# Kernel tuning notes

Measured on AMD Instinct MI355X. Metric: run time of the kernel, lower is better.

The kernel has to match this reference:

```python
import jax, jax.numpy as jnp
import numpy as np
import math

B, N, M, H = 4, 1024, 1024, 512
EPS = 1e-5


def _ln(x, g, b):
    m = jnp.mean(x, axis=-1, keepdims=True)
    v = jnp.mean((x - m) ** 2, axis=-1, keepdims=True)
    return (x - m) * jax.lax.rsqrt(v + EPS) * g + b


def _heads(x, h):
    b, s, Hh = x.shape
    return x.reshape(b, s, h, Hh // h).transpose(0, 2, 1, 3)  # [b,h,s,d]


def _merge(x):
    b, h, s, d = x.shape
    return x.transpose(0, 2, 1, 3).reshape(b, s, h * d)


def _sdpa(q, k, v):
    d = q.shape[-1]
    a = jax.nn.softmax(jnp.einsum('bhqd,bhkd->bhqk', q, k) / math.sqrt(d), axis=-1)
    return jnp.einsum('bhqk,bhkd->bhqd', a, v)


def _attn(key, value, query, Wk, Wv, Wq, Wf, bf, g, b, h):
    residual = query
    K = _heads(key @ Wk, h)
    V = _heads(value @ Wv, h)
    Q = _heads(query @ Wq, h)
    r = _merge(_sdpa(Q, K, V))
    r = jnp.concatenate([residual, r], axis=-1) @ Wf + bf
    return _ln(r + residual, g, b)


def _sc_attn(x, x2, Wk, Wv, Wq, Wf, bf, g, b, h=2):
    residual = x
    sK, sV, sQ = _heads(x @ Wk, h), _heads(x @ Wv, h), _heads(x @ Wq, h)
    cK, cV, cQ = _heads(x2 @ Wk, h), _heads(x2 @ Wv, h), _heads(x2 @ Wq, h)
    r = _sdpa(sQ, sK, sV) + _sdpa(cQ, cK, cV) + _sdpa(cQ, sK, sV) + _sdpa(sQ, cK, cV)
    r = _merge(r)
    r = jnp.concatenate([residual, r], axis=-1) @ Wf + bf
    return _ln(r + residual, g, b)


def _forward(context_x, context_y, target_x, in_W, in_b, cx_W, cx_b, tx_W, tx_b,
             sc_Wk, sc_Wv, sc_Wq, sc_Wf, sc_bf, sc_g, sc_b,
             ca_Wk, ca_Wv, ca_Wq, ca_Wf, ca_bf, ca_g, ca_b):
    bsz = context_x.shape[0]
    y = context_y.reshape(bsz, -1, 4, 2)
    proj = lambda yd: jnp.concatenate([context_x, yd], axis=-1) @ in_W + in_b
    e = proj(y[:, :, 0, :])
    e1 = proj(y[:, :, 1, :])
    e2 = proj(y[:, :, 2, :])
    e3 = proj(y[:, :, 3, :])
    # first self pass: key2/value2/query2 == current encoder_input
    for i in range(2):
        e = _sc_attn(e, e, sc_Wk[i], sc_Wv[i], sc_Wq[i], sc_Wf[i], sc_bf[i], sc_g[i], sc_b[i])
    for x2 in (e1, e2, e3):
        for i in range(2):
            e = _sc_attn(e, x2, sc_Wk[i], sc_Wv[i], sc_Wq[i], sc_Wf[i], sc_bf[i], sc_g[i], sc_b[i])
    q = target_x @ tx_W + tx_b
    k = context_x @ cx_W + cx_b
    for i in range(2):
        q = _attn(k, e, q, ca_Wk[i], ca_Wv[i], ca_Wq[i], ca_Wf[i], ca_bf[i], ca_g[i], ca_b[i], h=4)
    return q


def setup_inputs() -> dict:
    key = jax.random.key(0)
    ks = jax.random.split(key, 24)
    w = lambda i, shape, s: jax.random.normal(ks[i], shape, jnp.float32) * s
    return {
        'context_x': jax.random.normal(ks[0], (B, N, 1), jnp.float32),
        'context_y': jax.random.normal(ks[1], (B, N, 8), jnp.float32),
        'target_x': jax.random.normal(ks[2], (B, M, 1), jnp.float32),
        'in_W': w(3, (3, H), 0.5), 'in_b': jnp.zeros((H,), jnp.float32),
        'cx_W': w(4, (1, H), 0.5), 'cx_b': jnp.zeros((H,), jnp.float32),
        'tx_W': w(5, (1, H), 0.5), 'tx_b': jnp.zeros((H,), jnp.float32),
        'sc_Wk': w(6, (2, H, H), 0.03), 'sc_Wv': w(7, (2, H, H), 0.03), 'sc_Wq': w(8, (2, H, H), 0.03),
        'sc_Wf': w(9, (2, 2 * H, H), 0.03), 'sc_bf': jnp.zeros((2, H), jnp.float32),
        'sc_g': jnp.ones((2, H), jnp.float32), 'sc_b': jnp.zeros((2, H), jnp.float32),
        'ca_Wk': w(10, (2, H, H), 0.03), 'ca_Wv': w(11, (2, H, H), 0.03), 'ca_Wq': w(12, (2, H, H), 0.03),
        'ca_Wf': w(13, (2, 2 * H, H), 0.03), 'ca_bf': jnp.zeros((2, H), jnp.float32),
        'ca_g': jnp.ones((2, H), jnp.float32), 'ca_b': jnp.zeros((2, H), jnp.float32),
    }


def reference(context_x, context_y, target_x, in_W, in_b, cx_W, cx_b, tx_W, tx_b,
              sc_Wk, sc_Wv, sc_Wq, sc_Wf, sc_bf, sc_g, sc_b,
              ca_Wk, ca_Wv, ca_Wq, ca_Wf, ca_bf, ca_g, ca_b):
    return _forward(context_x, context_y, target_x, in_W, in_b, cx_W, cx_b, tx_W, tx_b,
                    sc_Wk, sc_Wv, sc_Wq, sc_Wf, sc_bf, sc_g, sc_b,
                    ca_Wk, ca_Wv, ca_Wq, ca_Wf, ca_bf, ca_g, ca_b)
```

## Files before the change

kernel.cpp:

```cpp
#include <hip/hip_runtime.h>

#define DEVINL __device__ __forceinline__

typedef short bf16x8 __attribute__((ext_vector_type(8)));
typedef float f32x4 __attribute__((ext_vector_type(4)));

#define LOG2E 1.44269504088896f

DEVINL unsigned f2b(float f) {
  unsigned u = __float_as_uint(f);
  u = (u + 0x7FFFu + ((u >> 16) & 1u)) >> 16;
  return u & 0xFFFFu;
}
DEVINL uint4 pack8(const float* v) {
  uint4 u;
  u.x = f2b(v[0]) | (f2b(v[1]) << 16);
  u.y = f2b(v[2]) | (f2b(v[3]) << 16);
  u.z = f2b(v[4]) | (f2b(v[5]) << 16);
  u.w = f2b(v[6]) | (f2b(v[7]) << 16);
  return u;
}

DEVINL float4 block_sum4(float4 v, float4* sh) {
  const int lane = threadIdx.x & 63, wid = threadIdx.x >> 6;
#pragma unroll
  for (int o = 32; o; o >>= 1) {
    v.x += __shfl_down(v.x, o);
    v.y += __shfl_down(v.y, o);
    v.z += __shfl_down(v.z, o);
    v.w += __shfl_down(v.w, o);
  }
  __syncthreads();
  if (lane == 0) sh[wid] = v;
  __syncthreads();
  float4 a = sh[0], b = sh[1], c = sh[2], d = sh[3], r;
  r.x = a.x + b.x + c.x + d.x;
  r.y = a.y + b.y + c.y + d.y;
  r.z = a.z + b.z + c.z + d.z;
  r.w = a.w + b.w + c.w + d.w;
  return r;
}
DEVINL float block_sum1(float v, float* sh) {
  const int lane = threadIdx.x & 63, wid = threadIdx.x >> 6;
#pragma unroll
  for (int o = 32; o; o >>= 1) v += __shfl_down(v, o);
  __syncthreads();
  if (lane == 0) sh[wid] = v;
  __syncthreads();
  return sh[0] + sh[1] + sh[2] + sh[3];
}

__global__ __launch_bounds__(256) void tabproj9_kernel(
    const float* __restrict__ in_W, const float* __restrict__ in_b,
    const float* __restrict__ cx_W, const float* __restrict__ cx_b,
    const float* __restrict__ tx_W, const float* __restrict__ tx_b,
    const float* __restrict__ sWk, const float* __restrict__ sWv,
    const float* __restrict__ sWq, const float* __restrict__ aWk,
    const float* __restrict__ aWq, float* __restrict__ Ttab) {
  const int z = blockIdx.y;
  const float* V;
  const float* bias;
  const float* W;
  float* P;
  int nvec;
  float scl = 1.f;
  if (z < 6) {
    V = in_W; bias = in_b; nvec = 3;
    const int i = z / 3, wsel = z % 3;
    W = (wsel == 0 ? sWk : wsel == 1 ? sWv : sWq) + (size_t)i * 262144;
    P = Ttab + (size_t)z * 2048;
    if (wsel == 2) scl = 0.0625f * LOG2E;
  } else if (z < 8) {
    V = cx_W; bias = cx_b; nvec = 1;
    W = aWk + (size_t)(z - 6) * 262144;
    P = Ttab + 12288 + (size_t)(z - 6) * 1024;
  } else {
    V = tx_W; bias = tx_b; nvec = 1;
    W = aWq; P = Ttab + 14336; scl = 0.08838834764831845f * LOG2E;
  }
  __shared__ float4 sh4[4];
  const int j = blockIdx.x, tid = threadIdx.x;
  float acc[4] = {0.f, 0.f, 0.f, 0.f};
  for (int kk = tid; kk < 512; kk += 256) {
    const float w = W[(size_t)kk * 512 + j];
    for (int v = 0; v < nvec; ++v) acc[v] += V[(size_t)v * 512 + kk] * w;
    acc[3] += bias[kk] * w;
  }
  float4 packed = make_float4(acc[0], acc[1], acc[2], acc[3]);
  packed = block_sum4(packed, sh4);
  if (tid == 0) {
    const float vals[4] = {packed.x * scl, packed.y * scl, packed.z * scl, packed.w * scl};
    for (int v = 0; v < nvec; ++v) P[(size_t)v * 512 + j] = vals[v];
    P[(size_t)nvec * 512 + j] = vals[3];
  }
}

__global__ __launch_bounds__(256) void transpose_kvq_kernel(
    const float* __restrict__ sWk, const float* __restrict__ sWv,
    const float* __restrict__ sWq, const float* __restrict__ aWv,
    const float* __restrict__ aWq, unsigned short* __restrict__ Wkvqt0,
    unsigned short* __restrict__ aWvt0, unsigned short* __restrict__ aWqt1) {
  const int z = blockIdx.z;
  const float* src;
  unsigned short* dst;
  float scl = 1.f;
  if (z < 6) {
    const int i = z / 3, wsel = z % 3;
    src = (wsel == 0 ? sWk : wsel == 1 ? sWv : sWq) + (size_t)i * 262144;
    dst = Wkvqt0 + (size_t)i * 786432 + (size_t)wsel * 262144;
    if (wsel == 2) scl = 0.0625f * LOG2E;
  } else if (z < 8) {
    src = aWv + (size_t)(z - 6) * 262144;
    dst = aWvt0 + (size_t)(z - 6) * 262144;
  } else {
    src = aWq + 262144; dst = aWqt1; scl = 0.08838834764831845f * LOG2E;
  }
  __shared__ float tile[32][33];
  const int n0 = blockIdx.x * 32, k0 = blockIdx.y * 32;
  const int tx = threadIdx.x, ty = threadIdx.y;
#pragma unroll
  for (int r = 0; r < 4; ++r)
    tile[ty + 8 * r][tx] = src[(size_t)(k0 + ty + 8 * r) * 512 + n0 + tx];
  __syncthreads();
#pragma unroll
  for (int r = 0; r < 4; ++r)
    dst[(size_t)(n0 + ty + 8 * r) * 512 + k0 + tx] =
        (unsigned short)f2b(scl * tile[tx][ty + 8 * r]);
}

__global__ __launch_bounds__(256) void transpose_f_kernel(
    const float* __restrict__ sWf, const float* __restrict__ aWf,
    unsigned short* __restrict__ Wft0, unsigned short* __restrict__ aWft0) {
  const int z = blockIdx.z;
  const float* src = (z < 2 ? sWf + (size_t)z * 524288 : aWf + (size_t)(z - 2) * 524288);
  unsigned short* dst =
      (z < 2 ? Wft0 + (size_t)z * 524288 : aWft0 + (size_t)(z - 2) * 524288);
  __shared__ float tile[32][33];
  const int n0 = blockIdx.x * 32, k0 = blockIdx.y * 32;
  const int tx = threadIdx.x, ty = threadIdx.y;
#pragma unroll
  for (int r = 0; r < 4; ++r)
    tile[ty + 8 * r][tx] = src[(size_t)(k0 + ty + 8 * r) * 512 + n0 + tx];
  __syncthreads();
#pragma unroll
  for (int r = 0; r < 4; ++r)
    dst[(size_t)(n0 + ty + 8 * r) * 1024 + k0 + tx] =
        (unsigned short)f2b(tile[tx][ty + 8 * r]);
}

__global__ __launch_bounds__(128) void affine3kq_kernel(
    const float* __restrict__ cx, const float* __restrict__ cy, int sel,
    const float* __restrict__ TK, const float* __restrict__ TQ,
    unsigned short* __restrict__ Kfr, unsigned short* __restrict__ Qbf) {
  const int row = blockIdx.x;
  const int b = row >> 10, s = row & 1023;
  const float x = cx[row];
  const float* y = cy + (size_t)row * 8 + 2 * sel;
  const float y0 = y[0], y1 = y[1];
  const int t = threadIdx.x;
  const bool isQ = t >= 64;
  const int c = t & 63;
  const int h = c >> 5;
  const int d0 = (c & 31) * 8;
  const float* T = isQ ? TQ : TK;
  float v[8];
#pragma unroll
  for (int j = 0; j < 8; ++j) {
    const int col = h * 256 + d0 + j;
    v[j] = x * T[col] + y0 * T[512 + col] + y1 * T[1024 + col] + T[1536 + col];
  }
  const uint4 u = pack8(v);
  const int bh = b * 2 + h;
  if (isQ) {
    *(uint4*)(Qbf + ((size_t)bh * 1024 + s) * 256 + d0) = u;
  } else {
    const int kc = d0 >> 5;
    const int lane = ((d0 & 31) >> 3) * 16 + (s & 15);
    *(uint4*)(Kfr + ((size_t)(bh * 8 + kc) * 64 + (s >> 4)) * 512 + lane * 8) = u;
  }
}

__global__ __launch_bounds__(256) void affine3v_frag_kernel(
    const float* __restrict__ cx, const float* __restrict__ cy, int sel,
    const float* __restrict__ TV, unsigned short* __restrict__ Vfr) {
  __shared__ float tile[32][33];
  const int s0 = blockIdx.x * 32, d0 = blockIdx.y * 32;
  const int bh = blockIdx.z;
  const int b = bh >> 1, h = bh & 1;
  const int tx = threadIdx.x, ty = threadIdx.y;
  const int col = h * 256 + d0 + tx;
  const float tv0 = TV[col], tv1 = TV[512 + col], tv2 = TV[1024 + col],
              tv3 = TV[1536 + col];
#pragma unroll
  for (int r = 0; r < 4; ++r) {
    const int row = b * 1024 + s0 + ty + 8 * r;
    const float x = cx[row];
    const float* y = cy + (size_t)row * 8 + 2 * sel;
    tile[ty + 8 * r][tx] = x * tv0 + y[0] * tv1 + y[1] * tv2 + tv3;
  }
  __syncthreads();
  const int idx = ty * 32 + tx;
  if (idx < 128) {
    const int dj = idx & 31, sch = idx >> 5;
    float v[8];
#pragma unroll
    for (int jj = 0; jj < 8; ++jj) v[jj] = tile[sch * 8 + jj][dj];
    const uint4 u = pack8(v);
    const int sc = s0 >> 5;
    const int dtile = (d0 + dj) >> 4;
    const int lane = sch * 16 + (dj & 15);
    *(uint4*)(Vfr + ((size_t)(bh * 32 + sc) * 16 + dtile) * 512 + lane * 8) = u;
  }
}

__global__ __launch_bounds__(64) void rank1_pack_kernel(
    const float* __restrict__ x, const float* __restrict__ T,
    unsigned short* __restrict__ dst, int isQ) {
  const int row = blockIdx.x;
  const int b = row >> 10, s = row & 1023;
  const float xv = x[row];
  const int c = threadIdx.x;
  const int h = c >> 4;
  const int d0 = (c & 15) * 8;
  float v[8];
#pragma unroll
  for (int j = 0; j < 8; ++j) {
    const int col = h * 128 + d0 + j;
    v[j] = xv * T[col] + T[512 + col];
  }
  const uint4 u = pack8(v);
  const int bh = b * 4 + h;
  if (isQ) {
    *(uint4*)(dst + ((size_t)bh * 1024 + s) * 128 + d0) = u;
  } else {
    const int kc = d0 >> 5;
    const int lane = ((d0 & 31) >> 3) * 16 + (s & 15);
    *(uint4*)(dst + ((size_t)(bh * 4 + kc) * 64 + (s >> 4)) * 512 + lane * 8) = u;
  }
}

__global__ __launch_bounds__(512) void affine3_kernel(
    const float* __restrict__ cx, const float* __restrict__ cy, int sel,
    const float* __restrict__ W3, const float* __restrict__ bias,
    float* __restrict__ out, unsigned short* __restrict__ outb) {
  const int r = blockIdx.x, j = threadIdx.x;
  const float* y = cy + (size_t)r * 8 + 2 * sel;
  const float v = cx[r] * W3[j] + y[0] * W3[512 + j] + y[1] * W3[1024 + j] + bias[j];
  if (out) out[(size_t)r * 512 + j] = v;
  if (outb) outb[(size_t)r * 512 + j] = (unsigned short)f2b(v);
}

__global__ __launch_bounds__(512) void rank1_kernel(
    const float* __restrict__ x, const float* __restrict__ w,
    const float* __restrict__ b, float* __restrict__ out,
    unsigned short* __restrict__ outb) {
  const int r = blockIdx.x, j = threadIdx.x;
  const float v = x[r] * w[j] + b[j];
  if (out) out[(size_t)r * 512 + j] = v;
  if (outb) outb[(size_t)r * 512 + j] = (unsigned short)f2b(v);
}

__global__ __launch_bounds__(256) void gemm_wf_kernel(
    const unsigned short* __restrict__ A0, const unsigned short* __restrict__ A1,
    const float* __restrict__ F0, const float* __restrict__ F1,
    const unsigned short* __restrict__ Wt, const float* __restrict__ bias,
    float* __restrict__ C0, float* __restrict__ C1) {
  constexpr int BM = 128, BN = 64, BK = 32, LDP = 40, K = 512, N = 512;
  __shared__ unsigned short As[2][BM * LDP];
  __shared__ unsigned short Bs[2][BN * LDP];
  const int kz = blockIdx.z;
  const int tid = threadIdx.x;
  const int lane = tid & 63, w = tid >> 6;
  const int bm = blockIdx.y * BM, bn = blockIdx.x * BN;
  const int wm = (w & 1) * 64, wn = (w >> 1) * 32;
  const int l15 = lane & 15, lq = lane >> 4;
  const int ar = tid >> 1, ac = (tid & 1) * 16;
  const int br = tid >> 2, bc = (tid & 3) * 8;
  const unsigned short* A = kz ? A1 : A0;
  const bool useF = (kz != 0) && (F0 != nullptr);
  const size_t arow = (size_t)(bm + ar) * 512;
  const size_t brow = (size_t)(bn + br) * 1024 + (size_t)kz * 512;
  f32x4 acc[4][2] = {};
  uint4 ra0, ra1, rb0;
#define GLOAD(k0_)                                                          \
  do {                                                                      \
    if (useF) {                                                             \
      const float* p0 = F0 + arow + (k0_) + ac;                             \
      const float* p1 = F1 + arow + (k0_) + ac;                             \
      float s[16];                                                          \
      const float4 x0 = *(const float4*)p0, x1 = *(const float4*)(p0 + 4);  \
      const float4 x2 = *(const float4*)(p0 + 8), x3 = *(const float4*)(p0 + 12); \
      const float4 y0 = *(const float4*)p1, y1 = *(const float4*)(p1 + 4);  \
      const float4 y2 = *(const float4*)(p1 + 8), y3 = *(const float4*)(p1 + 12); \
      s[0] = x0.x + y0.x; s[1] = x0.y + y0.y; s[2] = x0.z + y0.z; s[3] = x0.w + y0.w; \
      s[4] = x1.x + y1.x; s[5] = x1.y + y1.y; s[6] = x1.z + y1.z; s[7] = x1.w + y1.w; \
      s[8] = x2.x + y2.x; s[9] = x2.y + y2.y; s[10] = x2.z + y2.z; s[11] = x2.w + y2.w; \
      s[12] = x3.x + y3.x; s[13] = x3.y + y3.y; s[14] = x3.z + y3.z; s[15] = x3.w + y3.w; \
      ra0 = pack8(s); ra1 = pack8(s + 8);                                   \
    } else {                                                                \
      ra0 = *(const uint4*)(A + arow + (k0_) + ac);                         \
      ra1 = *(const uint4*)(A + arow + (k0_) + ac + 8);                     \
    }                                                                       \
    rb0 = *(const uint4*)(Wt + brow + (k0_) + bc);                          \
  } while (0)
  GLOAD(0);
  *(uint4*)(As[0] + ar * LDP + ac) = ra0;
  *(uint4*)(As[0] + ar * LDP + ac + 8) = ra1;
  *(uint4*)(Bs[0] + br * LDP + bc) = rb0;
  __syncthreads();
  int buf = 0;
  for (int k0 = 0; k0 < K; k0 += BK) {
    const bool more = (k0 + BK) < K;
    if (more) GLOAD(k0 + BK);
    bf16x8 af[4], bfr[2];
#pragma unroll
    for (int mt = 0; mt < 4; ++mt)
      af[mt] = *(const bf16x8*)(As[buf] + (wm + mt * 16 + l15) * LDP + lq * 8);
#pragma unroll
    for (int nt = 0; nt < 2; ++nt)
      bfr[nt] = *(const bf16x8*)(Bs[buf] + (wn + nt * 16 + l15) * LDP + lq * 8);
#pragma unroll
    for (int mt = 0; mt < 4; ++mt)
#pragma unroll
      for (int nt = 0; nt < 2; ++nt)
        acc[mt][nt] =
            __builtin_amdgcn_mfma_f32_16x16x32_bf16(af[mt], bfr[nt], acc[mt][nt], 0, 0, 0);
    if (more) {
      *(uint4*)(As[buf ^ 1] + ar * LDP + ac) = ra0;
      *(uint4*)(As[buf ^ 1] + ar * LDP + ac + 8) = ra1;
      *(uint4*)(Bs[buf ^ 1] + br * LDP + bc) = rb0;
    }
    __syncthreads();
    buf ^= 1;
  }
#undef GLOAD
  float* C = kz ? C1 : C0;
#pragma unroll
  for (int nt = 0; nt < 2; ++nt) {
    const int col = bn + wn + nt * 16 + l15;
    const float bv = (kz && bias) ? bias[col] : 0.f;
#pragma unroll
    for (int mt = 0; mt < 4; ++mt) {
#pragma unroll
      for (int r = 0; r < 4; ++r) {
        const int row = bm + wm + mt * 16 + lq * 4 + r;
        C[(size_t)row * N + col] = acc[mt][nt][r] + bv;
      }
    }
  }
}

template <int MODE>
__global__ __launch_bounds__(256) void gemm_pack_kernel(
    const unsigned short* __restrict__ A0, const unsigned short* __restrict__ Wt,
    unsigned short* __restrict__ Kfr, unsigned short* __restrict__ Vfr,
    unsigned short* __restrict__ Qbf) {
  constexpr int BM = 128, BN = 64, BK = 32, LDP = 40, K = 512;
  __shared__ unsigned short As[2][BM * LDP];
  __shared__ unsigned short Bs[2][BN * LDP];
  const int tid = threadIdx.x;
  const int lane = tid & 63, w = tid >> 6;
  const int bm = blockIdx.y * BM, bn = blockIdx.x * BN;
  const int wm = (w & 1) * 64, wn = (w >> 1) * 32;
  const int l15 = lane & 15, lq = lane >> 4;
  const int ar = tid >> 1, ac = (tid & 1) * 16;
  const int br = tid >> 2, bc = (tid & 3) * 8;
  f32x4 acc[4][2] = {};
  uint4 ra0 = *(const uint4*)(A0 + (size_t)(bm + ar) * K + ac);
  uint4 ra1 = *(const uint4*)(A0 + (size_t)(bm + ar) * K + ac + 8);
  uint4 rb0 = *(const uint4*)(Wt + (size_t)(bn + br) * K + bc);
  *(uint4*)(As[0] + ar * LDP + ac) = ra0;
  *(uint4*)(As[0] + ar * LDP + ac + 8) = ra1;
  *(uint4*)(Bs[0] + br * LDP + bc) = rb0;
  __syncthreads();
  int buf = 0;
  for (int k0 = 0; k0 < K; k0 += BK) {
    const bool more = (k0 + BK) < K;
    if (more) {
      ra0 = *(const uint4*)(A0 + (size_t)(bm + ar) * K + k0 + BK + ac);
      ra1 = *(const uint4*)(A0 + (size_t)(bm + ar) * K + k0 + BK + ac + 8);
      rb0 = *(const uint4*)(Wt + (size_t)(bn + br) * K + k0 + BK + bc);
    }
    bf16x8 af[4], bfr[2];
#pragma unroll
    for (int mt = 0; mt < 4; ++mt)
      af[mt] = *(const bf16x8*)(As[buf] + (wm + mt * 16 + l15) * LDP + lq * 8);
#pragma unroll
    for (int nt = 0; nt < 2; ++nt)
      bfr[nt] = *(const bf16x8*)(Bs[buf] + (wn + nt * 16 + l15) * LDP + lq * 8);
#pragma unroll
    for (int mt = 0; mt < 4; ++mt)
#pragma unroll
      for (int nt = 0; nt < 2; ++nt)
        acc[mt][nt] =
            __builtin_amdgcn_mfma_f32_16x16x32_bf16(af[mt], bfr[nt], acc[mt][nt], 0, 0, 0);
    if (more) {
      *(uint4*)(As[buf ^ 1] + ar * LDP + ac) = ra0;
      *(uint4*)(As[buf ^ 1] + ar * LDP + ac + 8) = ra1;
      *(uint4*)(Bs[buf ^ 1] + br * LDP + bc) = rb0;
    }
    __syncthreads();
    buf ^= 1;
  }
  const int b = bm >> 10;
  const int s0base = (bm & 1023) + wm + lq * 4;
#pragma unroll
  for (int nt = 0; nt < 2; ++nt) {
    const int col = bn + wn + nt * 16 + l15;
    int sec, h, d, nh2, Dv;
    if constexpr (MODE == 0) {
      sec = col >> 9; const int c = col & 511; h = c >> 8; d = c & 255; nh2 = 2; Dv = 256;
    } else if constexpr (MODE == 1) {
      sec = 1; h = col >> 7; d = col & 127; nh2 = 4; Dv = 128;
    } else {
      sec = 2; h = col >> 7; d = col & 127; nh2 = 4; Dv = 128;
    }
    const int bh = b * nh2 + h;
#pragma unroll
    for (int mt = 0; mt < 4; ++mt) {
      const int s0 = s0base + mt * 16;
      const float* a = (const float*)&acc[mt][nt];
      if (sec == 2) {
        unsigned short* q = Qbf + ((size_t)bh * 1024 + s0) * Dv + d;
#pragma unroll
        for (int r = 0; r < 4; ++r) q[(size_t)r * Dv] = (unsigned short)f2b(a[r]);
      } else if (sec == 0) {
        unsigned short* kp = Kfr +
            ((size_t)(bh * 8 + (d >> 5)) * 64 + (s0 >> 4)) * 512 +
            ((d & 31) >> 3) * 128 + (d & 7);
#pragma unroll
        for (int r = 0; r < 4; ++r)
          kp[((s0 & 15) + r) * 8] = (unsigned short)f2b(a[r]);
      } else {
        unsigned short* vp = Vfr +
            ((size_t)(bh * 32 + (s0 >> 5)) * (Dv / 16) + (d >> 4)) * 512 +
            (((s0 >> 3) & 3) * 16 + (d & 15)) * 8 + (s0 & 7);
        uint2 u;
        u.x = f2b(a[0]) | (f2b(a[1]) << 16);
        u.y = f2b(a[2]) | (f2b(a[3]) << 16);
        *(uint2*)vp = u;
      }
    }
  }
}

template <int D, int NKV>
__global__ __launch_bounds__(256, 2) void attn_mfma_kernel(
    const unsigned short* __restrict__ Qa, const unsigned short* __restrict__ Qb,
    const unsigned short* __restrict__ KfrA, const unsigned short* __restrict__ KfrB,
    const unsigned short* __restrict__ VfrA, const unsigned short* __restrict__ VfrB,
    float post_scale, int nh, unsigned short* __restrict__ R,
    float* __restrict__ Rp) {
  constexpr int NQS = NKV;
  constexpr int QP = D + 8;
  constexpr int WPh = 512 + 8;
  constexpr int DT = D / 64;
  const int tid = threadIdx.x;
  const int lane = tid & 63, w = tid >> 6;
  const int l15 = lane & 15, lq = lane >> 4;
  const int nbh = 4 * nh;
  int bx = blockIdx.x;
  int side = 0;
  if constexpr (NKV == 2) { side = bx >> 9; bx &= 511; }
  const int bh = bx % nbh;
  const int qb16 = (bx / nbh) * 16;
  const int b = bh / nh, head = bh % nh;
  const size_t rowb = (size_t)b * 1024;
  const int colo = head * D;

  __shared__ unsigned short qsh[NQS * 16 * QP];
  __shared__ unsigned short wsh[16 * WPh];
  __shared__ float redA[4][16];
  __shared__ float redB[4][16];

  for (int idx = tid; idx < NQS * 16 * (D / 8); idx += 256) {
    const int st = idx / (16 * (D / 8));
    const int rem = idx - st * 16 * (D / 8);
    const int r = rem / (D / 8), ch = rem - r * (D / 8);
    const unsigned short* Q = st ? Qb : Qa;
    const uint4 u = *(const uint4*)(Q + ((size_t)bh * 1024 + qb16 + r) * D + ch * 8);
    *(uint4*)(qsh + st * 16 * QP + r * QP + ch * 8) = u;
  }
  __syncthreads();

  const unsigned short* Kp = (side ? KfrB : KfrA) + (size_t)bh * ((size_t)D * 1024);
  const unsigned short* Vp = (side ? VfrB : VfrA) + (size_t)bh * ((size_t)D * 1024);

  f32x4 acc[NQS][16] = {};
#pragma unroll 1
  for (int kc = 0; kc < D / 32; ++kc) {
    bf16x8 kf[16];
#pragma unroll
    for (int st = 0; st < 16; ++st)
      kf[st] = *(const bf16x8*)(Kp + ((size_t)kc * 64 + w * 16 + st) * 512 + lane * 8);
    const bf16x8 qa = *(const bf16x8*)(qsh + l15 * QP + kc * 32 + lq * 8);
    __builtin_amdgcn_s_setprio(1);
#pragma unroll
    for (int st = 0; st < 16; ++st)
      acc[0][st] = __builtin_amdgcn_mfma_f32_16x16x32_bf16(qa, kf[st], acc[0][st], 0, 0, 0);
    __builtin_amdgcn_s_setprio(0);
    if constexpr (NQS == 2) {
      const bf16x8 qb2 = *(const bf16x8*)(qsh + 16 * QP + l15 * QP + kc * 32 + lq * 8);
      __builtin_amdgcn_s_setprio(1);
#pragma unroll
      for (int st = 0; st < 16; ++st)
        acc[1][st] =
            __builtin_amdgcn_mfma_f32_16x16x32_bf16(qb2, kf[st], acc[1][st], 0, 0, 0);
      __builtin_amdgcn_s_setprio(0);
    }
  }

  float psA[4] = {0.f, 0.f, 0.f, 0.f}, psB[4] = {0.f, 0.f, 0.f, 0.f};
#pragma unroll
  for (int st = 0; st < 16; ++st)
#pragma unroll
    for (int r = 0; r < 4; ++r) {
      acc[0][st][r] = exp2f(acc[0][st][r]);
      psA[r] += acc[0][st][r];
      if constexpr (NQS == 2) {
        acc[1][st][r] = exp2f(acc[1][st][r]);
        psB[r] += acc[1][st][r];
      }
    }
#pragma unroll
  for (int o = 1; o < 16; o <<= 1)
#pragma unroll
    for (int r = 0; r < 4; ++r) {
      psA[r] += __shfl_xor(psA[r], o);
      if constexpr (NQS == 2) psB[r] += __shfl_xor(psB[r], o);
    }
  if (l15 == 0) {
#pragma unroll
    for (int r = 0; r < 4; ++r) {
      redA[w][lq * 4 + r] = psA[r];
      if constexpr (NQS == 2) redB[w][lq * 4 + r] = psB[r];
    }
  }
  __syncthreads();
  float invA[4], invB[4];
#pragma unroll
  for (int r = 0; r < 4; ++r) {
    invA[r] = 1.f / (redA[0][lq * 4 + r] + redA[1][lq * 4 + r] +
                     redA[2][lq * 4 + r] + redA[3][lq * 4 + r]);
    if constexpr (NQS == 2)
      invB[r] = 1.f / (redB[0][lq * 4 + r] + redB[1][lq * 4 + r] +
                       redB[2][lq * 4 + r] + redB[3][lq * 4 + r]);
  }

  f32x4 acc_o[DT] = {};
#pragma unroll
  for (int half = 0; half < 2; ++half) {
#pragma unroll
    for (int st = 0; st < 8; ++st) {
      const int g = half * 8 + st;
#pragma unroll
      for (int r = 0; r < 4; ++r) {
        float wv = acc[0][g][r] * invA[r];
        if constexpr (NQS == 2) wv += acc[1][g][r] * invB[r];
        wsh[(lq * 4 + r) * WPh + w * 128 + st * 16 + l15] = (unsigned short)f2b(wv);
      }
    }
    __syncthreads();
#pragma unroll 1
    for (int sh2 = 0; sh2 < 16; sh2 += 2) {
      bf16x8 pa[2], vb[2][DT];
#pragma unroll
      for (int u = 0; u < 2; ++u) {
        const int sc = sh2 + u;
        pa[u] = *(const bf16x8*)(wsh + l15 * WPh + sc * 32 + lq * 8);
        const int scg = (sc >> 2) * 8 + half * 4 + (sc & 3);
#pragma unroll
        for (int dt = 0; dt < DT; ++dt)
          vb[u][dt] = *(const bf16x8*)(
              Vp + ((size_t)scg * (D / 16) + w * DT + dt) * 512 + lane * 8);
      }
      __builtin_amdgcn_s_setprio(1);
#pragma unroll
      for (int u = 0; u < 2; ++u)
#pragma unroll
        for (int dt = 0; dt < DT; ++dt)
          acc_o[dt] =
              __builtin_amdgcn_mfma_f32_16x16x32_bf16(pa[u], vb[u][dt], acc_o[dt], 0, 0, 0);
      __builtin_amdgcn_s_setprio(0);
    }
    __syncthreads();
  }

  if constexpr (NKV == 2) {
    float* dst = Rp + (size_t)side * (4096 * 512) + (rowb + qb16) * 512 + colo;
#pragma unroll
    for (int dt = 0; dt < DT; ++dt)
#pragma unroll
      for (int r = 0; r < 4; ++r) {
        const int q = lq * 4 + r;
        const int d = w * (DT * 16) + dt * 16 + l15;
        dst[(size_t)q * 512 + d] = acc_o[dt][r];
      }
  } else {
#pragma unroll
    for (int dt = 0; dt < DT; ++dt)
#pragma unroll
      for (int r = 0; r < 4; ++r) {
        const int q = lq * 4 + r;
        const int d = w * (DT * 16) + dt * 16 + l15;
        R[(rowb + qb16 + q) * 512 + colo + d] =
            (unsigned short)f2b(acc_o[dt][r] * post_scale);
      }
  }
}

__global__ __launch_bounds__(256) void ln_kernel(
    const float* __restrict__ G0, const float* __restrict__ G1,
    const float* __restrict__ res, const float* __restrict__ g,
    const float* __restrict__ b, float* __restrict__ out,
    unsigned short* __restrict__ outb) {
  __shared__ float sh[4];
  const int row = blockIdx.x, tid = threadIdx.x;
  const size_t off = (size_t)row * 512;
  const float x0 = G0[off + tid] + G1[off + tid] + res[off + tid];
  const float x1 = G0[off + tid + 256] + G1[off + tid + 256] + res[off + tid + 256];
  const float mean = block_sum1(x0 + x1, sh) * (1.0f / 512.0f);
  const float d0 = x0 - mean, d1 = x1 - mean;
  const float var = block_sum1(d0 * d0 + d1 * d1, sh) * (1.0f / 512.0f);
  const float inv = rsqrtf(var + 1e-5f);
  const float y0 = d0 * inv * g[tid] + b[tid];
  const float y1 = d1 * inv * g[tid + 256] + b[tid + 256];
  out[off + tid] = y0;
  out[off + tid + 256] = y1;
  if (outb) {
    outb[off + tid] = (unsigned short)f2b(y0);
    outb[off + tid + 256] = (unsigned short)f2b(y1);
  }
}

extern "C" void kernel_launch(void* const* d_in, const int* in_sizes, int n_in,
                              void* d_out, int out_size, void* d_ws, size_t ws_size,
                              hipStream_t stream) {
  typedef unsigned short ushort_t;
  const float* cx   = (const float*)d_in[0];
  const float* cy   = (const float*)d_in[1];
  const float* txp  = (const float*)d_in[2];
  const float* in_W = (const float*)d_in[3];
  const float* in_b = (const float*)d_in[4];
  const float* cx_W = (const float*)d_in[5];
  const float* cx_b = (const float*)d_in[6];
  const float* tx_W = (const float*)d_in[7];
  const float* tx_b = (const float*)d_in[8];
  const float* sWk  = (const float*)d_in[9];
  const float* sWv  = (const float*)d_in[10];
  const float* sWq  = (const float*)d_in[11];
  const float* sWf  = (const float*)d_in[12];
  const float* sbf  = (const float*)d_in[13];
  const float* sg   = (const float*)d_in[14];
  const float* sb   = (const float*)d_in[15];
  const float* aWk  = (const float*)d_in[16];
  const float* aWv  = (const float*)d_in[17];
  const float* aWq  = (const float*)d_in[18];
  const float* aWf  = (const float*)d_in[19];
  const float* abf  = (const float*)d_in[20];
  const float* ag   = (const float*)d_in[21];
  const float* ab   = (const float*)d_in[22];

  const size_t MB = 1024 * 1024;
  char* ws = (char*)d_ws;
  float*    E     = (float*)(ws + 0 * MB);
  ushort_t* Ebf   = (ushort_t*)(ws + 8 * MB);
  float*    QA    = (float*)(ws + 12 * MB);
  ushort_t* QAbf  = (ushort_t*)(ws + 20 * MB);
  ushort_t* Rbbf  = (ushort_t*)(ws + 24 * MB);
  float*    Rp    = (float*)(ws + 28 * MB);
  float*    G0    = (float*)(ws + 44 * MB);
  ushort_t* KfrA  = (ushort_t*)(ws + 52 * MB);
  ushort_t* VfrA  = (ushort_t*)(ws + 56 * MB);
  ushort_t* QbfA  = (ushort_t*)(ws + 60 * MB);
  ushort_t* KfrB  = (ushort_t*)(ws + 64 * MB);
  ushort_t* VfrB  = (ushort_t*)(ws + 68 * MB);
  ushort_t* QbfB  = (ushort_t*)(ws + 72 * MB);
  float*    G1    = (float*)(ws + 84 * MB);
  ushort_t* Wkvqt0 = (ushort_t*)(ws + 92 * MB);
  ushort_t* Wkvqt[2] = {Wkvqt0, Wkvqt0 + 786432};
  ushort_t* Wft0   = (ushort_t*)(ws + 95 * MB);
  ushort_t* Wft[2] = {Wft0, Wft0 + 524288};
  ushort_t* aWvt0  = (ushort_t*)(ws + 97 * MB);
  ushort_t* aWvt[2] = {aWvt0, aWvt0 + 262144};
  ushort_t* aWqt1  = (ushort_t*)(ws + 98 * MB);
  ushort_t* aWft0  = (ushort_t*)(ws + 99 * MB);
  ushort_t* aWft[2] = {aWft0, aWft0 + 524288};
  float*    Ttab   = (float*)(ws + 101 * MB);

  float* T_sc[2][3];
  for (int i = 0; i < 2; ++i)
    for (int w = 0; w < 3; ++w) T_sc[i][w] = Ttab + (size_t)(i * 3 + w) * 2048;
  float* T_cak[2] = {Ttab + 12288, Ttab + 12288 + 1024};
  float* T_caq0 = Ttab + 14336;

  const dim3 tb(32, 8);

  transpose_kvq_kernel<<<dim3(16, 16, 9), tb, 0, stream>>>(sWk, sWv, sWq, aWv, aWq,
                                                           Wkvqt0, aWvt0, aWqt1);
  transpose_f_kernel<<<dim3(16, 32, 4), tb, 0, stream>>>(sWf, aWf, Wft0, aWft0);
  tabproj9_kernel<<<dim3(512, 9), 256, 0, stream>>>(in_W, in_b, cx_W, cx_b, tx_W, tx_b,
                                                    sWk, sWv, sWq, aWk, aWq, Ttab);

  affine3_kernel<<<4096, 512, 0, stream>>>(cx, cy, 0, in_W, in_b, E, Ebf);
  rank1_kernel<<<4096, 512, 0, stream>>>(txp, tx_W, tx_b, QA, QAbf);

  for (int p = 0; p < 4; ++p) {
    for (int i = 0; i < 2; ++i) {
      gemm_pack_kernel<0><<<dim3(24, 32), 256, 0, stream>>>(Ebf, Wkvqt[i], KfrA, VfrA,
                                                            QbfA);
      const float* F0 = nullptr;
      const float* F1 = nullptr;
      if (p > 0) {
        affine3kq_kernel<<<4096, 128, 0, stream>>>(cx, cy, p, T_sc[i][0], T_sc[i][2],
                                                   KfrB, QbfB);
        affine3v_frag_kernel<<<dim3(32, 8, 8), tb, 0, stream>>>(cx, cy, p, T_sc[i][1],
                                                                VfrB);
        attn_mfma_kernel<256, 2><<<1024, 256, 0, stream>>>(
            QbfA, QbfB, KfrA, KfrB, VfrA, VfrB, 1.0f, 2, nullptr, Rp);
        F0 = Rp; F1 = Rp + 4096 * 512;
      } else {
        attn_mfma_kernel<256, 1><<<512, 256, 0, stream>>>(
            QbfA, QbfA, KfrA, KfrA, VfrA, VfrA, 4.0f, 2, Rbbf, nullptr);
      }
      gemm_wf_kernel<<<dim3(8, 32, 2), 256, 0, stream>>>(
          Ebf, Rbbf, F0, F1, Wft[i], sbf + (size_t)i * 512, G0, G1);
      ln_kernel<<<4096, 256, 0, stream>>>(G0, G1, E, sg + (size_t)i * 512,
                                          sb + (size_t)i * 512, E, Ebf);
    }
  }

  for (int i = 0; i < 2; ++i) {
    rank1_pack_kernel<<<4096, 64, 0, stream>>>(cx, T_cak[i], KfrA, 0);
    gemm_pack_kernel<1><<<dim3(8, 32), 256, 0, stream>>>(Ebf, aWvt[i], nullptr, VfrA,
                                                         nullptr);
    if (i == 0) {
      rank1_pack_kernel<<<4096, 64, 0, stream>>>(txp, T_caq0, QbfB, 1);
    } else {
      gemm_pack_kernel<2><<<dim3(8, 32), 256, 0, stream>>>(QAbf, aWqt1, nullptr, nullptr,
                                                           QbfB);
    }
    attn_mfma_kernel<128, 1><<<1024, 256, 0, stream>>>(
        QbfB, QbfB, KfrA, KfrA, VfrA, VfrA, 1.0f, 4, Rbbf, nullptr);
    gemm_wf_kernel<<<dim3(8, 32, 2), 256, 0, stream>>>(
        QAbf, Rbbf, nullptr, nullptr, aWft[i], abf + (size_t)i * 512, G0, G1);
    ln_kernel<<<4096, 256, 0, stream>>>(G0, G1, QA, ag + (size_t)i * 512,
                                        ab + (size_t)i * 512,
                                        (i == 1) ? (float*)d_out : QA,
                                        (i == 1) ? nullptr : QAbf);
  }
  (void)in_sizes; (void)n_in; (void)out_size; (void)ws_size;
}
```

Measured before the change: 1.064 ms.

## Restructure attention kernel into key-chunked loop with multi-tile query reuse

The attention kernel now walks the 1024 keys in four chunks, computing scores, exponentials and the P·V product per chunk. Probabilities are staged unnormalized in shared memory and normalized once at the end. The full score accumulator no longer has to stay in registers, and a new QT template parameter lets each block handle several 16-row query tiles, so each loaded K/V fragment is reused across more queries. In the two-side case the normalized outputs are summed in registers, and grid sizes are halved to match. The cost is more shared memory, more barriers per block, and fewer blocks in flight.

New measurement: 1.029 ms. 3.3% less time.

```diff
diff --git a/kernel.cpp b/kernel.cpp
--- a/kernel.cpp
+++ b/kernel.cpp
@@ -444,168 +444,185 @@
   }
 }
 
-template <int D, int NKV>
+template <int D, int NQS, int QT>
 __global__ __launch_bounds__(256, 2) void attn_mfma_kernel(
     const unsigned short* __restrict__ Qa, const unsigned short* __restrict__ Qb,
     const unsigned short* __restrict__ KfrA, const unsigned short* __restrict__ KfrB,
     const unsigned short* __restrict__ VfrA, const unsigned short* __restrict__ VfrB,
     float post_scale, int nh, unsigned short* __restrict__ R,
     float* __restrict__ Rp) {
-  constexpr int NQS = NKV;
   constexpr int QP = D + 8;
-  constexpr int WPh = 512 + 8;
+  constexpr int SP = 256 + 8;
   constexpr int DT = D / 64;
+  constexpr int NR = QT * 16;
   const int tid = threadIdx.x;
   const int lane = tid & 63, w = tid >> 6;
   const int l15 = lane & 15, lq = lane >> 4;
   const int nbh = 4 * nh;
   int bx = blockIdx.x;
   int side = 0;
-  if constexpr (NKV == 2) { side = bx >> 9; bx &= 511; }
+  if constexpr (NQS == 2) { side = bx >> 8; bx &= 255; }
   const int bh = bx % nbh;
-  const int qb16 = (bx / nbh) * 16;
+  const int qb = (bx / nbh) * NR;
   const int b = bh / nh, head = bh % nh;
   const size_t rowb = (size_t)b * 1024;
   const int colo = head * D;
 
-  __shared__ unsigned short qsh[NQS * 16 * QP];
-  __shared__ unsigned short wsh[16 * WPh];
-  __shared__ float redA[4][16];
-  __shared__ float redB[4][16];
-
-  for (int idx = tid; idx < NQS * 16 * (D / 8); idx += 256) {
-    const int st = idx / (16 * (D / 8));
-    const int rem = idx - st * 16 * (D / 8);
+  __shared__ unsigned short qsh[NQS * NR * QP];
+  __shared__ unsigned short ssh[NQS * NR * SP];
+  __shared__ float red[NQS * QT * 4 * 16];
+
+  for (int idx = tid; idx < NQS * NR * (D / 8); idx += 256) {
+    const int set = idx / (NR * (D / 8));
+    const int rem = idx - set * NR * (D / 8);
     const int r = rem / (D / 8), ch = rem - r * (D / 8);
-    const unsigned short* Q = st ? Qb : Qa;
-    const uint4 u = *(const uint4*)(Q + ((size_t)bh * 1024 + qb16 + r) * D + ch * 8);
-    *(uint4*)(qsh + st * 16 * QP + r * QP + ch * 8) = u;
+    const unsigned short* Q = set ? Qb : Qa;
+    const uint4 u = *(const uint4*)(Q + ((size_t)bh * 1024 + qb + r) * D + ch * 8);
+    *(uint4*)(qsh + (set * NR + r) * QP + ch * 8) = u;
   }
   __syncthreads();
 
   const unsigned short* Kp = (side ? KfrB : KfrA) + (size_t)bh * ((size_t)D * 1024);
   const unsigned short* Vp = (side ? VfrB : VfrA) + (size_t)bh * ((size_t)D * 1024);
 
-  f32x4 acc[NQS][16] = {};
+  float psum[QT][NQS][4];
+#pragma unroll
+  for (int qt = 0; qt < QT; ++qt)
+#pragma unroll
+    for (int s2 = 0; s2 < NQS; ++s2)
+#pragma unroll
+      for (int r = 0; r < 4; ++r) psum[qt][s2][r] = 0.f;
+  f32x4 acc_o[QT][NQS][DT] = {};
+
 #pragma unroll 1
-  for (int kc = 0; kc < D / 32; ++kc) {
-    bf16x8 kf[16];
-#pragma unroll
-    for (int st = 0; st < 16; ++st)
-      kf[st] = *(const bf16x8*)(Kp + ((size_t)kc * 64 + w * 16 + st) * 512 + lane * 8);
-    const bf16x8 qa = *(const bf16x8*)(qsh + l15 * QP + kc * 32 + lq * 8);
-    __builtin_amdgcn_s_setprio(1);
-#pragma unroll
-    for (int st = 0; st < 16; ++st)
-      acc[0][st] = __builtin_amdgcn_mfma_f32_16x16x32_bf16(qa, kf[st], acc[0][st], 0, 0, 0);
-    __builtin_amdgcn_s_setprio(0);
-    if constexpr (NQS == 2) {
-      const bf16x8 qb2 = *(const bf16x8*)(qsh + 16 * QP + l15 * QP + kc * 32 + lq * 8);
+  for (int c = 0; c < 4; ++c) {
+    f32x4 sacc[QT][NQS][4] = {};
+#pragma unroll 1
+    for (int kc = 0; kc < D / 32; ++kc) {
+      bf16x8 kf[4];
+#pragma unroll
+      for (int st = 0; st < 4; ++st)
+        kf[st] = *(const bf16x8*)(
+            Kp + ((size_t)kc * 64 + c * 16 + w * 4 + st) * 512 + lane * 8);
+      bf16x8 qf[QT][NQS];
+#pragma unroll
+      for (int qt = 0; qt < QT; ++qt)
+#pragma unroll
+        for (int s2 = 0; s2 < NQS; ++s2)
+          qf[qt][s2] = *(const bf16x8*)(
+              qsh + (s2 * NR + qt * 16 + l15) * QP + kc * 32 + lq * 8);
       __builtin_amdgcn_s_setprio(1);
 #pragma unroll
-      for (int st = 0; st < 16; ++st)
-        acc[1][st] =
-            __builtin_amdgcn_mfma_f32_16x16x32_bf16(qb2, kf[st], acc[1][st], 0, 0, 0);
+      for (int st = 0; st < 4; ++st)
+#pragma unroll
+        for (int qt = 0; qt < QT; ++qt)
+#pragma unroll
+          for (int s2 = 0; s2 < NQS; ++s2)
+            sacc[qt][s2][st] = __builtin_amdgcn_mfma_f32_16x16x32_bf16(
+                qf[qt][s2], kf[st], sacc[qt][s2][st], 0, 0, 0);
       __builtin_amdgcn_s_setprio(0);
     }
-  }
-
-  float psA[4] = {0.f, 0.f, 0.f, 0.f}, psB[4] = {0.f, 0.f, 0.f, 0.f};
-#pragma unroll
-  for (int st = 0; st < 16; ++st)
-#pragma unroll
-    for (int r = 0; r < 4; ++r) {
-      acc[0][st][r] = exp2f(acc[0][st][r]);
-      psA[r] += acc[0][st][r];
-      if constexpr (NQS == 2) {
-        acc[1][st][r] = exp2f(acc[1][st][r]);
-        psB[r] += acc[1][st][r];
-      }
-    }
-#pragma unroll
-  for (int o = 1; o < 16; o <<= 1)
-#pragma unroll
-    for (int r = 0; r < 4; ++r) {
-      psA[r] += __shfl_xor(psA[r], o);
-      if constexpr (NQS == 2) psB[r] += __shfl_xor(psB[r], o);
-    }
-  if (l15 == 0) {
-#pragma unroll
-    for (int r = 0; r < 4; ++r) {
-      redA[w][lq * 4 + r] = psA[r];
-      if constexpr (NQS == 2) redB[w][lq * 4 + r] = psB[r];
-    }
-  }
-  __syncthreads();
-  float invA[4], invB[4];
-#pragma unroll
-  for (int r = 0; r < 4; ++r) {
-    invA[r] = 1.f / (redA[0][lq * 4 + r] + redA[1][lq * 4 + r] +
-                     redA[2][lq * 4 + r] + redA[3][lq * 4 + r]);
-    if constexpr (NQS == 2)
-      invB[r] = 1.f / (redB[0][lq * 4 + r] + redB[1][lq * 4 + r] +
-                       redB[2][lq * 4 + r] + redB[3][lq * 4 + r]);
-  }
-
-  f32x4 acc_o[DT] = {};
-#pragma unroll
-  for (int half = 0; half < 2; ++half) {
-#pragma unroll
-    for (int st = 0; st < 8; ++st) {
-      const int g = half * 8 + st;
-#pragma unroll
-      for (int r = 0; r < 4; ++r) {
-        float wv = acc[0][g][r] * invA[r];
-        if constexpr (NQS == 2) wv += acc[1][g][r] * invB[r];
-        wsh[(lq * 4 + r) * WPh + w * 128 + st * 16 + l15] = (unsigned short)f2b(wv);
-      }
-    }
+#pragma unroll
+    for (int qt = 0; qt < QT; ++qt)
+#pragma unroll
+      for (int s2 = 0; s2 < NQS; ++s2)
+#pragma unroll
+        for (int st = 0; st < 4; ++st)
+#pragma unroll
+          for (int r = 0; r < 4; ++r) {
+            const float e = exp2f(sacc[qt][s2][st][r]);
+            psum[qt][s2][r] += e;
+            ssh[(s2 * NR + qt * 16 + lq * 4 + r) * SP + (w * 4 + st) * 16 + l15] =
+                (unsigned short)f2b(e);
+          }
     __syncthreads();
 #pragma unroll 1
-    for (int sh2 = 0; sh2 < 16; sh2 += 2) {
-      bf16x8 pa[2], vb[2][DT];
+    for (int sc = 0; sc < 8; sc += 2) {
+      bf16x8 vb[2][DT], pa[2][QT][NQS];
 #pragma unroll
       for (int u = 0; u < 2; ++u) {
-        const int sc = sh2 + u;
-        pa[u] = *(const bf16x8*)(wsh + l15 * WPh + sc * 32 + lq * 8);
-        const int scg = (sc >> 2) * 8 + half * 4 + (sc & 3);
 #pragma unroll
         for (int dt = 0; dt < DT; ++dt)
           vb[u][dt] = *(const bf16x8*)(
-              Vp + ((size_t)scg * (D / 16) + w * DT + dt) * 512 + lane * 8);
+              Vp + ((size_t)(c * 8 + sc + u) * (D / 16) + w * DT + dt) * 512 + lane * 8);
+#pragma unroll
+        for (int qt = 0; qt < QT; ++qt)
+#pragma unroll
+          for (int s2 = 0; s2 < NQS; ++s2)
+            pa[u][qt][s2] = *(const bf16x8*)(
+                ssh + (s2 * NR + qt * 16 + l15) * SP + (sc + u) * 32 + lq * 8);
       }
       __builtin_amdgcn_s_setprio(1);
 #pragma unroll
       for (int u = 0; u < 2; ++u)
 #pragma unroll
-        for (int dt = 0; dt < DT; ++dt)
-          acc_o[dt] =
-              __builtin_amdgcn_mfma_f32_16x16x32_bf16(pa[u], vb[u][dt], acc_o[dt], 0, 0, 0);
+        for (int qt = 0; qt < QT; ++qt)
+#pragma unroll
+          for (int s2 = 0; s2 < NQS; ++s2)
+#pragma unroll
+            for (int dt = 0; dt < DT; ++dt)
+              acc_o[qt][s2][dt] = __builtin_amdgcn_mfma_f32_16x16x32_bf16(
+                  pa[u][qt][s2], vb[u][dt], acc_o[qt][s2][dt], 0, 0, 0);
       __builtin_amdgcn_s_setprio(0);
     }
     __syncthreads();
   }
 
-  if constexpr (NKV == 2) {
-    float* dst = Rp + (size_t)side * (4096 * 512) + (rowb + qb16) * 512 + colo;
-#pragma unroll
-    for (int dt = 0; dt < DT; ++dt)
+#pragma unroll
+  for (int o = 1; o < 16; o <<= 1)
+#pragma unroll
+    for (int qt = 0; qt < QT; ++qt)
+#pragma unroll
+      for (int s2 = 0; s2 < NQS; ++s2)
+#pragma unroll
+        for (int r = 0; r < 4; ++r)
+          psum[qt][s2][r] += __shfl_xor(psum[qt][s2][r], o);
+  if (l15 == 0) {
+#pragma unroll
+    for (int qt = 0; qt < QT; ++qt)
+#pragma unroll
+      for (int s2 = 0; s2 < NQS; ++s2)
+#pragma unroll
+        for (int r = 0; r < 4; ++r)
+          red[((s2 * QT + qt) * 4 + w) * 16 + lq * 4 + r] = psum[qt][s2][r];
+  }
+  __syncthreads();
+  float inv[QT][NQS][4];
+#pragma unroll
+  for (int qt = 0; qt < QT; ++qt)
+#pragma unroll
+    for (int s2 = 0; s2 < NQS; ++s2)
 #pragma unroll
       for (int r = 0; r < 4; ++r) {
-        const int q = lq * 4 + r;
-        const int d = w * (DT * 16) + dt * 16 + l15;
-        dst[(size_t)q * 512 + d] = acc_o[dt][r];
+        const float* rp = red + ((s2 * QT + qt) * 4) * 16 + lq * 4 + r;
+        inv[qt][s2][r] = 1.f / (rp[0] + rp[16] + rp[32] + rp[48]);
       }
+
+  if constexpr (NQS == 2) {
+    float* base = Rp + (size_t)side * (4096 * 512);
+#pragma unroll
+    for (int qt = 0; qt < QT; ++qt)
+#pragma unroll
+      for (int dt = 0; dt < DT; ++dt)
+#pragma unroll
+        for (int r = 0; r < 4; ++r) {
+          const int q = qb + qt * 16 + lq * 4 + r;
+          const int d = w * (DT * 16) + dt * 16 + l15;
+          base[(rowb + q) * 512 + colo + d] =
+              acc_o[qt][0][dt][r] * inv[qt][0][r] + acc_o[qt][1][dt][r] * inv[qt][1][r];
+        }
   } else {
 #pragma unroll
-    for (int dt = 0; dt < DT; ++dt)
-#pragma unroll
-      for (int r = 0; r < 4; ++r) {
-        const int q = lq * 4 + r;
-        const int d = w * (DT * 16) + dt * 16 + l15;
-        R[(rowb + qb16 + q) * 512 + colo + d] =
-            (unsigned short)f2b(acc_o[dt][r] * post_scale);
-      }
+    for (int qt = 0; qt < QT; ++qt)
+#pragma unroll
+      for (int dt = 0; dt < DT; ++dt)
+#pragma unroll
+        for (int r = 0; r < 4; ++r) {
+          const int q = qb + qt * 16 + lq * 4 + r;
+          const int d = w * (DT * 16) + dt * 16 + l15;
+          R[(rowb + q) * 512 + colo + d] =
+              (unsigned short)f2b(acc_o[qt][0][dt][r] * inv[qt][0][r] * post_scale);
+        }
   }
 }
 
@@ -716,11 +733,11 @@
                                                    KfrB, QbfB);
         affine3v_frag_kernel<<<dim3(32, 8, 8), tb, 0, stream>>>(cx, cy, p, T_sc[i][1],
                                                                 VfrB);
-        attn_mfma_kernel<256, 2><<<1024, 256, 0, stream>>>(
+        attn_mfma_kernel<256, 2, 2><<<512, 256, 0, stream>>>(
             QbfA, QbfB, KfrA, KfrB, VfrA, VfrB, 1.0f, 2, nullptr, Rp);
         F0 = Rp; F1 = Rp + 4096 * 512;
       } else {
-        attn_mfma_kernel<256, 1><<<512, 256, 0, stream>>>(
+        attn_mfma_kernel<256, 1, 1><<<512, 256, 0, stream>>>(
             QbfA, QbfA, KfrA, KfrA, VfrA, VfrA, 4.0f, 2, Rbbf, nullptr);
       }
       gemm_wf_kernel<<<dim3(8, 32, 2), 256, 0, stream>>>(
@@ -740,7 +757,7 @@
       gemm_pack_kernel<2><<<dim3(8, 32), 256, 0, stream>>>(QAbf, aWqt1, nullptr, nullptr,
                                                            QbfB);
     }
-    attn_mfma_kernel<128, 1><<<1024, 256, 0, stream>>>(
+    attn_mfma_kernel<128, 1, 2><<<512, 256, 0, stream>>>(
         QbfB, QbfB, KfrA, KfrA, VfrA, VfrA, 1.0f, 4, Rbbf, nullptr);
     gemm_wf_kernel<<<dim3(8, 32, 2), 256, 0, stream>>>(
         QAbf, Rbbf, nullptr, nullptr, aWft[i], abf + (size_t)i * 512, G0, G1);
```
